# Kernel optimization log

Measured on AMD Instinct MI355X. Metric: run time of the kernel, lower is better.

## Reference

```python
import jax, jax.numpy as jnp
import numpy as np

B = 8192
D = 626
TEMP = 0.25
EPS = 1e-8


def setup_inputs() -> dict:
    key = jax.random.key(0)
    k1, k2 = jax.random.split(key)
    anchors = jax.random.normal(k1, (B, D), dtype=jnp.float32)
    poss = jax.random.normal(k2, (B, D), dtype=jnp.float32)
    return {"anchors": anchors, "poss": poss}


def reference(anchors, poss):
    # Full pairwise cosine similarity: S[i, j] = cos(anchors[i], poss[j]).
    # torch.nn.CosineSimilarity: dot(x, y) / max(||x|| * ||y||, eps)
    na = jnp.linalg.norm(anchors, axis=1)          # [B]
    np_ = jnp.linalg.norm(poss, axis=1)            # [B]
    dots = anchors @ poss.T                        # [B, B]
    S = dots / jnp.maximum(na[:, None] * np_[None, :], EPS)

    diag = jnp.diagonal(S)                         # [B] positive-pair cosines
    logits = S / TEMP
    # loss_i = -log( exp(logits_ii) / sum_j exp(logits_ij) )
    loss = jax.nn.logsumexp(logits, axis=1) - jnp.diagonal(logits)

    n = S.shape[0]
    cos_an_pos = diag.mean()
    cos_an_neg = ((S.sum(axis=1) - diag) / (n - 1)).mean()
    return (loss.mean(), cos_an_pos, cos_an_neg)
```

## Files before the change

### kernel.cpp

```cpp
#include <hip/hip_runtime.h>
#include <stdint.h>

#define B_N   8192
#define D_K   626
#define KPAD  640
#define BK    128
#define KSTEPS 5
#define BM    128
#define BN    128
#define COL_CHUNKS 16
#define TILES_PER_CHUNK 4
#define FIN_BLOCKS 16

typedef __attribute__((ext_vector_type(4))) float f32x4;
typedef __attribute__((ext_vector_type(2))) long long2v;

__device__ __forceinline__ void async16(const unsigned char* g, unsigned char* l) {
    __builtin_amdgcn_global_load_lds(
        (const __attribute__((address_space(1))) unsigned int*)(const void*)g,
        (__attribute__((address_space(3))) unsigned int*)(void*)l,
        16, 0, 0);
}

__global__ __launch_bounds__(256) void normalize_kernel(
    const float* __restrict__ A, const float* __restrict__ P,
    unsigned char* __restrict__ Af8, unsigned char* __restrict__ Pf8,
    float* __restrict__ rowexp, float* __restrict__ rowsum, float* __restrict__ acc)
{
    const int which = blockIdx.y;
    const float* srcM = which ? P : A;
    unsigned char* dstM = which ? Pf8 : Af8;
    const int t  = threadIdx.x;
    const int wv = t >> 6;
    const int L  = t & 63;
    const int rowBase = blockIdx.x * 32 + wv * 8;

    if (which == 0) {
        const int rb = blockIdx.x * 32;
        if (t < 32) { rowexp[rb + t] = 0.0f; rowsum[rb + t] = 0.0f; }
        if (blockIdx.x == 0 && t < 4) acc[t] = 0.0f;
    }

    #pragma unroll 2
    for (int j = 0; j < 8; ++j) {
        const int r = rowBase + j;
        const float2* s2 = (const float2*)(srcM + (size_t)r * D_K);

        float2 a0 = s2[2 * L];       float2 a1 = s2[2 * L + 1];
        float2 b0 = s2[2 * L + 128]; float2 b1 = s2[2 * L + 129];
        float2 c0 = {0.f, 0.f},      c1 = {0.f, 0.f};
        if (L < 28)       { c0 = s2[2 * L + 256]; c1 = s2[2 * L + 257]; }
        else if (L == 28) { c0 = s2[312]; }

        float ss = a0.x * a0.x + a0.y * a0.y + a1.x * a1.x + a1.y * a1.y
                 + b0.x * b0.x + b0.y * b0.y + b1.x * b1.x + b1.y * b1.y
                 + c0.x * c0.x + c0.y * c0.y + c1.x * c1.x + c1.y * c1.y;
        #pragma unroll
        for (int off = 32; off; off >>= 1) ss += __shfl_xor(ss, off, 64);
        const float rn = rsqrtf(ss);

        int* d4 = (int*)(dstM + (size_t)r * KPAD);
        int pk0 = __builtin_amdgcn_cvt_pk_fp8_f32(a0.x * rn, a0.y * rn, 0, false);
        pk0 = __builtin_amdgcn_cvt_pk_fp8_f32(a1.x * rn, a1.y * rn, pk0, true);
        d4[L] = pk0;
        int pk1 = __builtin_amdgcn_cvt_pk_fp8_f32(b0.x * rn, b0.y * rn, 0, false);
        pk1 = __builtin_amdgcn_cvt_pk_fp8_f32(b1.x * rn, b1.y * rn, pk1, true);
        d4[L + 64] = pk1;
        if (L < 32) {
            int pk2 = __builtin_amdgcn_cvt_pk_fp8_f32(c0.x * rn, c0.y * rn, 0, false);
            pk2 = __builtin_amdgcn_cvt_pk_fp8_f32(c1.x * rn, c1.y * rn, pk2, true);
            d4[L + 128] = pk2;
        }
    }
}

__global__ __launch_bounds__(256, 2) void gemm_fused_kernel(
    const unsigned char* __restrict__ Af8, const unsigned char* __restrict__ Pf8,
    float* __restrict__ rowexp, float* __restrict__ rowsum, float* __restrict__ diag)
{
    __shared__ __align__(16) unsigned char sA[2][BM * BK];
    __shared__ __align__(16) unsigned char sB[2][BN * BK];

    const int t    = threadIdx.x;
    const int lane = t & 63;
    const int w    = t >> 6;
    const int wr   = w >> 1;
    const int wc   = w & 1;
    const int quad = lane >> 4;
    const int l15  = lane & 15;
    const int rx   = l15 & 7;

    const int rowBase = blockIdx.x * BM;
    const int chunk   = blockIdx.y;

    const int p0 = t, p1 = t + 256, p2 = t + 512, p3 = t + 768;
    const int r0 = p0 >> 3, r1 = p1 >> 3, r2 = p2 >> 3, r3 = p3 >> 3;
    const size_t g0 = (size_t)r0 * KPAD + (size_t)(((p0 & 7) ^ (r0 & 7)) * 16);
    const size_t g1 = (size_t)r1 * KPAD + (size_t)(((p1 & 7) ^ (r1 & 7)) * 16);
    const size_t g2 = (size_t)r2 * KPAD + (size_t)(((p2 & 7) ^ (r2 & 7)) * 16);
    const size_t g3 = (size_t)r3 * KPAD + (size_t)(((p3 & 7) ^ (r3 & 7)) * 16);

    const unsigned char* Ab = Af8 + (size_t)rowBase * KPAD;
    const unsigned char* PbChunk = Pf8 + (size_t)(chunk * TILES_PER_CHUNK) * BN * KPAD;

    const int aRow = wr * 64 + l15;
    const int bRow = wc * 64 + l15;
    const int cOff0 = ((quad) ^ rx) * 16;
    const int cOff1 = ((4 + quad) ^ rx) * 16;

    float psum[4][4], pexp[4][4];
    #pragma unroll
    for (int i = 0; i < 4; ++i)
        #pragma unroll
        for (int j = 0; j < 4; ++j) { psum[i][j] = 0.0f; pexp[i][j] = 0.0f; }

    f32x4 acc[4][4];
    const f32x4 z = {0.f, 0.f, 0.f, 0.f};
    #pragma unroll
    for (int i = 0; i < 4; ++i)
        #pragma unroll
        for (int j = 0; j < 4; ++j) acc[i][j] = z;

    {
        async16(Ab + g0, &sA[0][p0 * 16]);
        async16(Ab + g1, &sA[0][p1 * 16]);
        async16(Ab + g2, &sA[0][p2 * 16]);
        async16(Ab + g3, &sA[0][p3 * 16]);
        async16(PbChunk + g0, &sB[0][p0 * 16]);
        async16(PbChunk + g1, &sB[0][p1 * 16]);
        async16(PbChunk + g2, &sB[0][p2 * 16]);
        async16(PbChunk + g3, &sB[0][p3 * 16]);
    }

    int par = 0;
    for (int ct = 0; ct < TILES_PER_CHUNK; ++ct) {
        #pragma unroll 1
        for (int ks = 0; ks < KSTEPS; ++ks) {
            __syncthreads();

            int nks = ks + 1, nct = ct;
            if (nks == KSTEPS) { nks = 0; ++nct; }
            if (nct < TILES_PER_CHUNK) {
                const int nxt = par ^ 1;
                const size_t nkOff = (size_t)nks * BK;
                const unsigned char* PbN = PbChunk + (size_t)nct * BN * KPAD + nkOff;
                const unsigned char* AbN = Ab + nkOff;
                async16(AbN + g0, &sA[nxt][p0 * 16]);
                async16(AbN + g1, &sA[nxt][p1 * 16]);
                async16(AbN + g2, &sA[nxt][p2 * 16]);
                async16(AbN + g3, &sA[nxt][p3 * 16]);
                async16(PbN + g0, &sB[nxt][p0 * 16]);
                async16(PbN + g1, &sB[nxt][p1 * 16]);
                async16(PbN + g2, &sB[nxt][p2 * 16]);
                async16(PbN + g3, &sB[nxt][p3 * 16]);
            }

            #pragma unroll
            for (int p = 0; p < 2; ++p) {
                const int cOff = p ? cOff1 : cOff0;
                long2v aF[4], bF[4];
                #pragma unroll
                for (int mi = 0; mi < 4; ++mi)
                    aF[mi] = *(const long2v*)&sA[par][(aRow + mi * 16) * BK + cOff];
                #pragma unroll
                for (int ni = 0; ni < 4; ++ni)
                    bF[ni] = *(const long2v*)&sB[par][(bRow + ni * 16) * BK + cOff];

                #pragma unroll
                for (int half = 0; half < 2; ++half)
                    #pragma unroll
                    for (int mi = 0; mi < 4; ++mi)
                        #pragma unroll
                        for (int ni = 0; ni < 4; ++ni)
                            acc[mi][ni] = __builtin_amdgcn_mfma_f32_16x16x32_fp8_fp8(
                                aF[mi][half], bF[ni][half], acc[mi][ni], 0, 0, 0);
            }
            par ^= 1;
        }

        const int colBase = (chunk * TILES_PER_CHUNK + ct) * BN;

        if (rowBase == colBase && wr == wc) {
            #pragma unroll
            for (int mi = 0; mi < 4; ++mi)
                #pragma unroll
                for (int r = 0; r < 4; ++r)
                    if (l15 == quad * 4 + r)
                        diag[rowBase + wr * 64 + mi * 16 + l15] = acc[mi][mi][r];
        }

        #pragma unroll
        for (int mi = 0; mi < 4; ++mi) {
            #pragma unroll
            for (int r = 0; r < 4; ++r) {
                float s4 = 0.f, e4 = 0.f;
                #pragma unroll
                for (int ni = 0; ni < 4; ++ni) {
                    const float S = acc[mi][ni][r];
                    s4 += S;
                    e4 += __expf(S * 4.0f);
                }
                psum[mi][r] += s4;
                pexp[mi][r] += e4;
            }
        }
        #pragma unroll
        for (int i = 0; i < 4; ++i)
            #pragma unroll
            for (int j = 0; j < 4; ++j) acc[i][j] = z;
    }

    #pragma unroll
    for (int off = 1; off <= 8; off <<= 1) {
        #pragma unroll
        for (int mi = 0; mi < 4; ++mi)
            #pragma unroll
            for (int r = 0; r < 4; ++r) {
                psum[mi][r] += __shfl_xor(psum[mi][r], off, 64);
                pexp[mi][r] += __shfl_xor(pexp[mi][r], off, 64);
            }
    }
    if (l15 == 0) {
        #pragma unroll
        for (int mi = 0; mi < 4; ++mi)
            #pragma unroll
            for (int r = 0; r < 4; ++r) {
                const int gr = rowBase + wr * 64 + mi * 16 + quad * 4 + r;
                atomicAdd(&rowsum[gr], psum[mi][r]);
                atomicAdd(&rowexp[gr], pexp[mi][r]);
            }
    }
}

__global__ __launch_bounds__(256) void finalize_kernel(
    const float* __restrict__ rowexp, const float* __restrict__ rowsum,
    const float* __restrict__ diag, float* __restrict__ acc, float* __restrict__ out)
{
    const int t = threadIdx.x;
    float ls = 0.f, ds = 0.f, ns = 0.f;
    for (int i = blockIdx.x * 256 + t; i < B_N; i += FIN_BLOCKS * 256) {
        const float d = diag[i];
        ls += __logf(rowexp[i]) - d * 4.0f;
        ds += d;
        ns += (rowsum[i] - d);
    }
    #pragma unroll
    for (int off = 32; off; off >>= 1) {
        ls += __shfl_down(ls, off, 64);
        ds += __shfl_down(ds, off, 64);
        ns += __shfl_down(ns, off, 64);
    }
    __shared__ float sl[4], sd[4], sn[4];
    if ((t & 63) == 0) { sl[t >> 6] = ls; sd[t >> 6] = ds; sn[t >> 6] = ns; }
    __syncthreads();
    if (t == 0) {
        atomicAdd(acc + 0, sl[0] + sl[1] + sl[2] + sl[3]);
        atomicAdd(acc + 1, sd[0] + sd[1] + sd[2] + sd[3]);
        atomicAdd(acc + 2, sn[0] + sn[1] + sn[2] + sn[3]);
        __threadfence();
        const int done = (int)atomicAdd((unsigned int*)(acc + 3), 1u);
        if (done == FIN_BLOCKS - 1) {
            const float L  = atomicAdd(acc + 0, 0.0f);
            const float Dm = atomicAdd(acc + 1, 0.0f);
            const float Nn = atomicAdd(acc + 2, 0.0f);
            out[0] = L / (float)B_N;
            out[1] = Dm / (float)B_N;
            out[2] = (Nn / (float)(B_N - 1)) / (float)B_N;
        }
    }
}

__global__ __launch_bounds__(256) void fb_norm(
    const float* __restrict__ A, const float* __restrict__ P,
    float* __restrict__ rna, float* __restrict__ rnp, float* __restrict__ acc)
{
    const int r = blockIdx.x;
    const float* src = blockIdx.y ? P : A;
    const int t = threadIdx.x;
    float ss = 0.f;
    for (int k = t; k < D_K; k += 256) { float v = src[(size_t)r * D_K + k]; ss += v * v; }
    #pragma unroll
    for (int off = 32; off; off >>= 1) ss += __shfl_down(ss, off, 64);
    __shared__ float sred[4];
    if ((t & 63) == 0) sred[t >> 6] = ss;
    __syncthreads();
    if (t == 0) {
        const float rn = rsqrtf(sred[0] + sred[1] + sred[2] + sred[3]);
        (blockIdx.y ? rnp : rna)[r] = rn;
    }
    if (blockIdx.x == 0 && blockIdx.y == 0 && t < 3) acc[t] = 0.0f;
}

__global__ __launch_bounds__(256) void fb_main(
    const float* __restrict__ A, const float* __restrict__ P,
    const float* __restrict__ rna, const float* __restrict__ rnp,
    float* __restrict__ acc)
{
    __shared__ float sa[D_K];
    __shared__ float red[12];
    const int i = blockIdx.x;
    const int t = threadIdx.x;
    const float rn = rna[i];
    for (int k = t; k < D_K; k += 256) sa[k] = A[(size_t)i * D_K + k] * rn;
    __syncthreads();
    const int w = t >> 6, lane = t & 63;
    float we = 0.f, wsum = 0.f, wd = 0.f;
    for (int j = w; j < B_N; j += 4) {
        float dot = 0.f;
        const float* p = P + (size_t)j * D_K;
        for (int k = lane; k < D_K; k += 64) dot += sa[k] * p[k];
        #pragma unroll
        for (int off = 32; off; off >>= 1) dot += __shfl_xor(dot, off, 64);
        const float S = dot * rnp[j];
        we += __expf(S * 4.0f);
        wsum += S;
        if (j == i) wd = S;
    }
    if (lane == 0) { red[w] = we; red[4 + w] = wsum; red[8 + w] = wd; }
    __syncthreads();
    if (t == 0) {
        const float E  = red[0] + red[1] + red[2] + red[3];
        const float Sm = red[4] + red[5] + red[6] + red[7];
        const float Dd = red[8] + red[9] + red[10] + red[11];
        atomicAdd(acc + 0, __logf(E) - 4.0f * Dd);
        atomicAdd(acc + 1, Dd);
        atomicAdd(acc + 2, Sm - Dd);
    }
}

__global__ void fb_fin(const float* __restrict__ acc, float* __restrict__ out)
{
    out[0] = acc[0] / (float)B_N;
    out[1] = acc[1] / (float)B_N;
    out[2] = acc[2] / ((float)(B_N - 1) * (float)B_N);
}

extern "C" void kernel_launch(void* const* d_in, const int* in_sizes, int n_in,
                              void* d_out, int out_size, void* d_ws, size_t ws_size,
                              hipStream_t stream)
{
    const float* A = (const float*)d_in[0];
    const float* P = (const float*)d_in[1];
    float* out = (float*)d_out;
    char* ws = (char*)d_ws;

    const size_t AF8_OFF  = 0;
    const size_t PF8_OFF  = AF8_OFF + (size_t)B_N * KPAD;
    const size_t REXP_OFF = PF8_OFF + (size_t)B_N * KPAD;
    const size_t RSUM_OFF = REXP_OFF + (size_t)B_N * sizeof(float);
    const size_t DIAG_OFF = RSUM_OFF + (size_t)B_N * sizeof(float);
    const size_t ACC_OFF  = DIAG_OFF + (size_t)B_N * sizeof(float);
    const size_t MAIN_REQ = ACC_OFF + 16;

    if (ws_size >= MAIN_REQ) {
        unsigned char* Af8 = (unsigned char*)(ws + AF8_OFF);
        unsigned char* Pf8 = (unsigned char*)(ws + PF8_OFF);
        float* rowexp = (float*)(ws + REXP_OFF);
        float* rowsum = (float*)(ws + RSUM_OFF);
        float* diag   = (float*)(ws + DIAG_OFF);
        float* acc    = (float*)(ws + ACC_OFF);

        normalize_kernel<<<dim3(B_N / 32, 2), 256, 0, stream>>>(A, P, Af8, Pf8,
                                                                rowexp, rowsum, acc);
        gemm_fused_kernel<<<dim3(B_N / BM, COL_CHUNKS), 256, 0, stream>>>(
            Af8, Pf8, rowexp, rowsum, diag);
        finalize_kernel<<<FIN_BLOCKS, 256, 0, stream>>>(rowexp, rowsum, diag, acc, out);
    } else {
        float* rna = (float*)ws;
        float* rnp = rna + B_N;
        float* acc = rnp + B_N;
        fb_norm<<<dim3(B_N, 2), 256, 0, stream>>>(A, P, rna, rnp, acc);
        fb_main<<<B_N, 256, 0, stream>>>(A, P, rna, rnp, acc);
        fb_fin<<<1, 1, 0, stream>>>(acc, out);
    }
}
```

Baseline: 156.9 us.

## Halve GEMM K-tile to raise occupancy and fuse finalize into last-block epilogue

```diff
diff --git a/kernel.cpp b/kernel.cpp
--- a/kernel.cpp
+++ b/kernel.cpp
@@ -4,13 +4,13 @@
 #define B_N   8192
 #define D_K   626
 #define KPAD  640
-#define BK    128
-#define KSTEPS 5
+#define BK    64
+#define KSTEPS 10
 #define BM    128
 #define BN    128
 #define COL_CHUNKS 16
 #define TILES_PER_CHUNK 4
-#define FIN_BLOCKS 16
+#define GRID_BLOCKS (B_N / BM * COL_CHUNKS)
 
 typedef __attribute__((ext_vector_type(4))) float f32x4;
 typedef __attribute__((ext_vector_type(2))) long long2v;
@@ -74,12 +74,15 @@
     }
 }
 
-__global__ __launch_bounds__(256, 2) void gemm_fused_kernel(
+__global__ __launch_bounds__(256, 4) void gemm_fused_kernel(
     const unsigned char* __restrict__ Af8, const unsigned char* __restrict__ Pf8,
-    float* __restrict__ rowexp, float* __restrict__ rowsum, float* __restrict__ diag)
+    float* __restrict__ rowexp, float* __restrict__ rowsum, float* __restrict__ diag,
+    float* __restrict__ acc4, float* __restrict__ out)
 {
     __shared__ __align__(16) unsigned char sA[2][BM * BK];
     __shared__ __align__(16) unsigned char sB[2][BN * BK];
+    __shared__ int lastFlag;
+    __shared__ float sl[4], sd[4], sn[4];
 
     const int t    = threadIdx.x;
     const int lane = t & 63;
@@ -88,25 +91,26 @@
     const int wc   = w & 1;
     const int quad = lane >> 4;
     const int l15  = lane & 15;
-    const int rx   = l15 & 7;
 
     const int rowBase = blockIdx.x * BM;
     const int chunk   = blockIdx.y;
 
-    const int p0 = t, p1 = t + 256, p2 = t + 512, p3 = t + 768;
-    const int r0 = p0 >> 3, r1 = p1 >> 3, r2 = p2 >> 3, r3 = p3 >> 3;
-    const size_t g0 = (size_t)r0 * KPAD + (size_t)(((p0 & 7) ^ (r0 & 7)) * 16);
-    const size_t g1 = (size_t)r1 * KPAD + (size_t)(((p1 & 7) ^ (r1 & 7)) * 16);
-    const size_t g2 = (size_t)r2 * KPAD + (size_t)(((p2 & 7) ^ (r2 & 7)) * 16);
-    const size_t g3 = (size_t)r3 * KPAD + (size_t)(((p3 & 7) ^ (r3 & 7)) * 16);
+    const int p0 = t, p1 = t + 256;
+    const int r0 = p0 >> 2, r1 = p1 >> 2;
+    const int sw0 = (r0 & 3) ^ ((r0 >> 2) & 3);
+    const int sw1 = (r1 & 3) ^ ((r1 >> 2) & 3);
+    const size_t g0 = (size_t)r0 * KPAD + (size_t)(((p0 & 3) ^ sw0) * 16);
+    const size_t g1 = (size_t)r1 * KPAD + (size_t)(((p1 & 3) ^ sw1) * 16);
 
     const unsigned char* Ab = Af8 + (size_t)rowBase * KPAD;
     const unsigned char* PbChunk = Pf8 + (size_t)(chunk * TILES_PER_CHUNK) * BN * KPAD;
 
     const int aRow = wr * 64 + l15;
     const int bRow = wc * 64 + l15;
-    const int cOff0 = ((quad) ^ rx) * 16;
-    const int cOff1 = ((4 + quad) ^ rx) * 16;
+    const int swA = (aRow & 3) ^ ((aRow >> 2) & 3);
+    const int swB = (bRow & 3) ^ ((bRow >> 2) & 3);
+    const int cOffA = ((quad ^ swA) * 16);
+    const int cOffB = ((quad ^ swB) * 16);
 
     float psum[4][4], pexp[4][4];
     #pragma unroll
@@ -121,20 +125,14 @@
         #pragma unroll
         for (int j = 0; j < 4; ++j) acc[i][j] = z;
 
-    {
-        async16(Ab + g0, &sA[0][p0 * 16]);
-        async16(Ab + g1, &sA[0][p1 * 16]);
-        async16(Ab + g2, &sA[0][p2 * 16]);
-        async16(Ab + g3, &sA[0][p3 * 16]);
-        async16(PbChunk + g0, &sB[0][p0 * 16]);
-        async16(PbChunk + g1, &sB[0][p1 * 16]);
-        async16(PbChunk + g2, &sB[0][p2 * 16]);
-        async16(PbChunk + g3, &sB[0][p3 * 16]);
-    }
+    async16(Ab + g0, &sA[0][p0 * 16]);
+    async16(Ab + g1, &sA[0][p1 * 16]);
+    async16(PbChunk + g0, &sB[0][p0 * 16]);
+    async16(PbChunk + g1, &sB[0][p1 * 16]);
 
     int par = 0;
     for (int ct = 0; ct < TILES_PER_CHUNK; ++ct) {
-        #pragma unroll 1
+        #pragma unroll 2
         for (int ks = 0; ks < KSTEPS; ++ks) {
             __syncthreads();
 
@@ -147,34 +145,26 @@
                 const unsigned char* AbN = Ab + nkOff;
                 async16(AbN + g0, &sA[nxt][p0 * 16]);
                 async16(AbN + g1, &sA[nxt][p1 * 16]);
-                async16(AbN + g2, &sA[nxt][p2 * 16]);
-                async16(AbN + g3, &sA[nxt][p3 * 16]);
                 async16(PbN + g0, &sB[nxt][p0 * 16]);
                 async16(PbN + g1, &sB[nxt][p1 * 16]);
-                async16(PbN + g2, &sB[nxt][p2 * 16]);
-                async16(PbN + g3, &sB[nxt][p3 * 16]);
             }
 
-            #pragma unroll
-            for (int p = 0; p < 2; ++p) {
-                const int cOff = p ? cOff1 : cOff0;
-                long2v aF[4], bF[4];
+            long2v aF[4], bF[4];
+            #pragma unroll
+            for (int mi = 0; mi < 4; ++mi)
+                aF[mi] = *(const long2v*)&sA[par][(aRow + mi * 16) * BK + cOffA];
+            #pragma unroll
+            for (int ni = 0; ni < 4; ++ni)
+                bF[ni] = *(const long2v*)&sB[par][(bRow + ni * 16) * BK + cOffB];
+
+            #pragma unroll
+            for (int half = 0; half < 2; ++half)
                 #pragma unroll
                 for (int mi = 0; mi < 4; ++mi)
-                    aF[mi] = *(const long2v*)&sA[par][(aRow + mi * 16) * BK + cOff];
-                #pragma unroll
-                for (int ni = 0; ni < 4; ++ni)
-                    bF[ni] = *(const long2v*)&sB[par][(bRow + ni * 16) * BK + cOff];
-
-                #pragma unroll
-                for (int half = 0; half < 2; ++half)
                     #pragma unroll
-                    for (int mi = 0; mi < 4; ++mi)
-                        #pragma unroll
-                        for (int ni = 0; ni < 4; ++ni)
-                            acc[mi][ni] = __builtin_amdgcn_mfma_f32_16x16x32_fp8_fp8(
-                                aF[mi][half], bF[ni][half], acc[mi][ni], 0, 0, 0);
-            }
+                    for (int ni = 0; ni < 4; ++ni)
+                        acc[mi][ni] = __builtin_amdgcn_mfma_f32_16x16x32_fp8_fp8(
+                            aF[mi][half], bF[ni][half], acc[mi][ni], 0, 0, 0);
             par ^= 1;
         }
 
@@ -186,7 +176,8 @@
                 #pragma unroll
                 for (int r = 0; r < 4; ++r)
                     if (l15 == quad * 4 + r)
-                        diag[rowBase + wr * 64 + mi * 16 + l15] = acc[mi][mi][r];
+                        atomicExch(&diag[rowBase + wr * 64 + mi * 16 + l15],
+                                   acc[mi][mi][r]);
         }
 
         #pragma unroll
@@ -230,39 +221,35 @@
                 atomicAdd(&rowexp[gr], pexp[mi][r]);
             }
     }
-}
-
-__global__ __launch_bounds__(256) void finalize_kernel(
-    const float* __restrict__ rowexp, const float* __restrict__ rowsum,
-    const float* __restrict__ diag, float* __restrict__ acc, float* __restrict__ out)
-{
-    const int t = threadIdx.x;
-    float ls = 0.f, ds = 0.f, ns = 0.f;
-    for (int i = blockIdx.x * 256 + t; i < B_N; i += FIN_BLOCKS * 256) {
-        const float d = diag[i];
-        ls += __logf(rowexp[i]) - d * 4.0f;
-        ds += d;
-        ns += (rowsum[i] - d);
-    }
-    #pragma unroll
-    for (int off = 32; off; off >>= 1) {
-        ls += __shfl_down(ls, off, 64);
-        ds += __shfl_down(ds, off, 64);
-        ns += __shfl_down(ns, off, 64);
-    }
-    __shared__ float sl[4], sd[4], sn[4];
-    if ((t & 63) == 0) { sl[t >> 6] = ls; sd[t >> 6] = ds; sn[t >> 6] = ns; }
+
+    __threadfence();
+    if (t == 0) {
+        const unsigned int done = atomicAdd((unsigned int*)(acc4 + 3), 1u);
+        lastFlag = (done == (unsigned int)(GRID_BLOCKS - 1));
+    }
     __syncthreads();
-    if (t == 0) {
-        atomicAdd(acc + 0, sl[0] + sl[1] + sl[2] + sl[3]);
-        atomicAdd(acc + 1, sd[0] + sd[1] + sd[2] + sd[3]);
-        atomicAdd(acc + 2, sn[0] + sn[1] + sn[2] + sn[3]);
-        __threadfence();
-        const int done = (int)atomicAdd((unsigned int*)(acc + 3), 1u);
-        if (done == FIN_BLOCKS - 1) {
-            const float L  = atomicAdd(acc + 0, 0.0f);
-            const float Dm = atomicAdd(acc + 1, 0.0f);
-            const float Nn = atomicAdd(acc + 2, 0.0f);
+    if (lastFlag) {
+        float ls = 0.f, ds = 0.f, ns = 0.f;
+        for (int i = t; i < B_N; i += 256) {
+            const float e = atomicAdd(&rowexp[i], 0.0f);
+            const float s = atomicAdd(&rowsum[i], 0.0f);
+            const float d = atomicAdd(&diag[i], 0.0f);
+            ls += __logf(e) - d * 4.0f;
+            ds += d;
+            ns += (s - d);
+        }
+        #pragma unroll
+        for (int off = 32; off; off >>= 1) {
+            ls += __shfl_down(ls, off, 64);
+            ds += __shfl_down(ds, off, 64);
+            ns += __shfl_down(ns, off, 64);
+        }
+        if ((t & 63) == 0) { sl[t >> 6] = ls; sd[t >> 6] = ds; sn[t >> 6] = ns; }
+        __syncthreads();
+        if (t == 0) {
+            const float L  = sl[0] + sl[1] + sl[2] + sl[3];
+            const float Dm = sd[0] + sd[1] + sd[2] + sd[3];
+            const float Nn = sn[0] + sn[1] + sn[2] + sn[3];
             out[0] = L / (float)B_N;
             out[1] = Dm / (float)B_N;
             out[2] = (Nn / (float)(B_N - 1)) / (float)B_N;
@@ -363,8 +350,7 @@
         normalize_kernel<<<dim3(B_N / 32, 2), 256, 0, stream>>>(A, P, Af8, Pf8,
                                                                 rowexp, rowsum, acc);
         gemm_fused_kernel<<<dim3(B_N / BM, COL_CHUNKS), 256, 0, stream>>>(
-            Af8, Pf8, rowexp, rowsum, diag);
-        finalize_kernel<<<FIN_BLOCKS, 256, 0, stream>>>(rowexp, rowsum, diag, acc, out);
+            Af8, Pf8, rowexp, rowsum, diag, acc, out);
     } else {
         float* rna = (float*)ws;
         float* rnp = rna + B_N;
```

Result: slower. 335.8 us (+114.1%).

## Load A fragments directly from global memory into registers, dropping A LDS tile

Applied to the files above, without the earlier changes.

```diff
diff --git a/kernel.cpp b/kernel.cpp
--- a/kernel.cpp
+++ b/kernel.cpp
@@ -74,11 +74,10 @@
     }
 }
 
-__global__ __launch_bounds__(256, 2) void gemm_fused_kernel(
+__global__ __launch_bounds__(256) void gemm_fused_kernel(
     const unsigned char* __restrict__ Af8, const unsigned char* __restrict__ Pf8,
     float* __restrict__ rowexp, float* __restrict__ rowsum, float* __restrict__ diag)
 {
-    __shared__ __align__(16) unsigned char sA[2][BM * BK];
     __shared__ __align__(16) unsigned char sB[2][BN * BK];
 
     const int t    = threadIdx.x;
@@ -100,10 +99,14 @@
     const size_t g2 = (size_t)r2 * KPAD + (size_t)(((p2 & 7) ^ (r2 & 7)) * 16);
     const size_t g3 = (size_t)r3 * KPAD + (size_t)(((p3 & 7) ^ (r3 & 7)) * 16);
 
-    const unsigned char* Ab = Af8 + (size_t)rowBase * KPAD;
     const unsigned char* PbChunk = Pf8 + (size_t)(chunk * TILES_PER_CHUNK) * BN * KPAD;
 
     const int aRow = wr * 64 + l15;
+    const unsigned char* aP[4];
+    #pragma unroll
+    for (int mi = 0; mi < 4; ++mi)
+        aP[mi] = Af8 + (size_t)(rowBase + aRow + mi * 16) * KPAD + quad * 16;
+
     const int bRow = wc * 64 + l15;
     const int cOff0 = ((quad) ^ rx) * 16;
     const int cOff1 = ((4 + quad) ^ rx) * 16;
@@ -121,51 +124,42 @@
         #pragma unroll
         for (int j = 0; j < 4; ++j) acc[i][j] = z;
 
-    {
-        async16(Ab + g0, &sA[0][p0 * 16]);
-        async16(Ab + g1, &sA[0][p1 * 16]);
-        async16(Ab + g2, &sA[0][p2 * 16]);
-        async16(Ab + g3, &sA[0][p3 * 16]);
-        async16(PbChunk + g0, &sB[0][p0 * 16]);
-        async16(PbChunk + g1, &sB[0][p1 * 16]);
-        async16(PbChunk + g2, &sB[0][p2 * 16]);
-        async16(PbChunk + g3, &sB[0][p3 * 16]);
-    }
+    async16(PbChunk + g0, &sB[0][p0 * 16]);
+    async16(PbChunk + g1, &sB[0][p1 * 16]);
+    async16(PbChunk + g2, &sB[0][p2 * 16]);
+    async16(PbChunk + g3, &sB[0][p3 * 16]);
 
     int par = 0;
     for (int ct = 0; ct < TILES_PER_CHUNK; ++ct) {
         #pragma unroll 1
         for (int ks = 0; ks < KSTEPS; ++ks) {
+            const int kOff = ks * BK;
             __syncthreads();
 
             int nks = ks + 1, nct = ct;
             if (nks == KSTEPS) { nks = 0; ++nct; }
             if (nct < TILES_PER_CHUNK) {
                 const int nxt = par ^ 1;
-                const size_t nkOff = (size_t)nks * BK;
-                const unsigned char* PbN = PbChunk + (size_t)nct * BN * KPAD + nkOff;
-                const unsigned char* AbN = Ab + nkOff;
-                async16(AbN + g0, &sA[nxt][p0 * 16]);
-                async16(AbN + g1, &sA[nxt][p1 * 16]);
-                async16(AbN + g2, &sA[nxt][p2 * 16]);
-                async16(AbN + g3, &sA[nxt][p3 * 16]);
+                const unsigned char* PbN =
+                    PbChunk + (size_t)nct * BN * KPAD + (size_t)nks * BK;
                 async16(PbN + g0, &sB[nxt][p0 * 16]);
                 async16(PbN + g1, &sB[nxt][p1 * 16]);
                 async16(PbN + g2, &sB[nxt][p2 * 16]);
                 async16(PbN + g3, &sB[nxt][p3 * 16]);
             }
 
-            #pragma unroll
-            for (int p = 0; p < 2; ++p) {
-                const int cOff = p ? cOff1 : cOff0;
-                long2v aF[4], bF[4];
-                #pragma unroll
-                for (int mi = 0; mi < 4; ++mi)
-                    aF[mi] = *(const long2v*)&sA[par][(aRow + mi * 16) * BK + cOff];
+            long2v aF0[4], aF1[4];
+            #pragma unroll
+            for (int mi = 0; mi < 4; ++mi) {
+                aF0[mi] = *(const long2v*)(aP[mi] + kOff);
+                aF1[mi] = *(const long2v*)(aP[mi] + kOff + 64);
+            }
+
+            {
+                long2v bF[4];
                 #pragma unroll
                 for (int ni = 0; ni < 4; ++ni)
-                    bF[ni] = *(const long2v*)&sB[par][(bRow + ni * 16) * BK + cOff];
-
+                    bF[ni] = *(const long2v*)&sB[par][(bRow + ni * 16) * BK + cOff0];
                 #pragma unroll
                 for (int half = 0; half < 2; ++half)
                     #pragma unroll
@@ -173,7 +167,21 @@
                         #pragma unroll
                         for (int ni = 0; ni < 4; ++ni)
                             acc[mi][ni] = __builtin_amdgcn_mfma_f32_16x16x32_fp8_fp8(
-                                aF[mi][half], bF[ni][half], acc[mi][ni], 0, 0, 0);
+                                aF0[mi][half], bF[ni][half], acc[mi][ni], 0, 0, 0);
+            }
+            {
+                long2v bF[4];
+                #pragma unroll
+                for (int ni = 0; ni < 4; ++ni)
+                    bF[ni] = *(const long2v*)&sB[par][(bRow + ni * 16) * BK + cOff1];
+                #pragma unroll
+                for (int half = 0; half < 2; ++half)
+                    #pragma unroll
+                    for (int mi = 0; mi < 4; ++mi)
+                        #pragma unroll
+                        for (int ni = 0; ni < 4; ++ni)
+                            acc[mi][ni] = __builtin_amdgcn_mfma_f32_16x16x32_fp8_fp8(
+                                aF1[mi][half], bF[ni][half], acc[mi][ni], 0, 0, 0);
             }
             par ^= 1;
         }
```

After: 245.2 us. 1.56x slower.
